# Optimization experiments

Hardware: AMD Instinct MI355X
Metric: run time of the kernel (lower is better)

Reference implementation:

```python
import jax, jax.numpy as jnp
import numpy as np

N_NODES = 50000
N_EDGES = 800000
NFEAT, NHID, IN_HEAD, NCLASS, OUT_HEAD = 256, 16, 8, 47, 1
NEG_SLOPE = 0.2


def setup_inputs() -> dict:
    key = jax.random.key(0)
    ks = jax.random.split(key, 10)
    x = jax.random.normal(ks[0], (N_NODES, NFEAT), dtype=jnp.float32)
    edge_index = jax.random.randint(ks[1], (2, N_EDGES), 0, N_NODES, dtype=jnp.int64)
    W1 = jax.random.normal(ks[2], (NFEAT, IN_HEAD * NHID), dtype=jnp.float32) * 0.06
    a1_src = jax.random.normal(ks[3], (IN_HEAD, NHID), dtype=jnp.float32) * 0.25
    a1_dst = jax.random.normal(ks[4], (IN_HEAD, NHID), dtype=jnp.float32) * 0.25
    b1 = jax.random.normal(ks[5], (IN_HEAD * NHID,), dtype=jnp.float32) * 0.02
    W2 = jax.random.normal(ks[6], (IN_HEAD * NHID, NCLASS), dtype=jnp.float32) * 0.09
    a2_src = jax.random.normal(ks[7], (OUT_HEAD, NCLASS), dtype=jnp.float32) * 0.15
    a2_dst = jax.random.normal(ks[8], (OUT_HEAD, NCLASS), dtype=jnp.float32) * 0.15
    b2 = jax.random.normal(ks[9], (NCLASS,), dtype=jnp.float32) * 0.02
    return {"x": x, "edge_index": edge_index, "W1": W1, "a1_src": a1_src,
            "a1_dst": a1_dst, "b1": b1, "W2": W2, "a2_src": a2_src,
            "a2_dst": a2_dst, "b2": b2}


def _gat_layer(x, W, a_src, a_dst, b, src, dst, n_nodes, concat):
    # x: [N, F_in]; W: [F_in, H*C]; a_*: [H, C]
    H, C = a_src.shape
    h = (x @ W).reshape(n_nodes, H, C)                        # [N, H, C]
    # per-node partial attention logits, then gather per edge
    s_src = jnp.einsum('nhc,hc->nh', h, a_src)                # [N, H]
    s_dst = jnp.einsum('nhc,hc->nh', h, a_dst)                # [N, H]
    e = jax.nn.leaky_relu(s_src[src] + s_dst[dst], NEG_SLOPE) # [E, H]
    # segment softmax over destination node
    m = jax.ops.segment_max(e, dst, num_segments=n_nodes)     # [N, H]
    ex = jnp.exp(e - m[dst])
    denom = jax.ops.segment_sum(ex, dst, num_segments=n_nodes)
    alpha = ex / (denom[dst] + 1e-16)                         # [E, H]
    # weighted message aggregation (scatter-add)
    msg = alpha[:, :, None] * h[src]                          # [E, H, C]
    out = jax.ops.segment_sum(msg, dst, num_segments=n_nodes) # [N, H, C]
    out = out.reshape(n_nodes, H * C) if concat else out.mean(axis=1)
    return out + b


def reference(x, edge_index, W1, a1_src, a1_dst, b1, W2, a2_src, a2_dst, b2):
    n = x.shape[0]
    # PyG GATConv default: add self-loops
    loops = jnp.arange(n, dtype=edge_index.dtype)
    src = jnp.concatenate([edge_index[0], loops])
    dst = jnp.concatenate([edge_index[1], loops])
    # eval mode: dropout is identity
    h = _gat_layer(x, W1, a1_src, a1_dst, b1, src, dst, n, concat=True)
    h = jax.nn.elu(h)
    out = _gat_layer(h, W2, a2_src, a2_dst, b2, src, dst, n, concat=False)
    return jax.nn.log_softmax(out, axis=1)
```

## Files before the change

### kernel.cpp

```cpp
#include <hip/hip_runtime.h>
#include <hip/hip_fp16.h>

#define N_NODES 50000
#define N_EDGES 800000
#define E2 (N_EDGES + N_NODES)

#define BSHIFT 6
#define BMASK 63
#define NBUCK 782
#define EPB 2048
#define NBLKC 416

typedef _Float16 h8v __attribute__((ext_vector_type(8)));
typedef float f4v __attribute__((ext_vector_type(4)));


__global__ __launch_bounds__(256) void k_hist(const int* __restrict__ ei,
        int* __restrict__ gh, const float* __restrict__ W1, _Float16* __restrict__ W1T,
        int* __restrict__ flag) {
    if (blockIdx.x == NBLKC) {
        if (threadIdx.x == 0) *flag = 0;
        for (int i = threadIdx.x; i < 128 * 256; i += 256) {
            int c = i >> 8, k = i & 255;
            W1T[i] = (_Float16)W1[k * 128 + c];
        }
        return;
    }
    __shared__ int h[NBUCK];
    int tid = threadIdx.x;
    for (int b = tid; b < NBUCK; b += 256) h[b] = 0;
    __syncthreads();
    int base = blockIdx.x * EPB;
    for (int i = tid; i < EPB; i += 256) {
        int e = base + i;
        if (e < E2) {
            int dst = (e < N_EDGES) ? ei[N_EDGES + e] : (e - N_EDGES);
            atomicAdd(&h[dst >> BSHIFT], 1);
        }
    }
    __syncthreads();
    for (int b = tid; b < NBUCK; b += 256) gh[blockIdx.x * NBUCK + b] = h[b];
}

__global__ __launch_bounds__(256) void k_colscan(int* __restrict__ gh,
        int* __restrict__ tot, int* __restrict__ boff, int* __restrict__ flag,
        const float* __restrict__ W2, float* __restrict__ W2p) {
    __shared__ int s_last;
    __shared__ int ws2[4];
    int wave = threadIdx.x >> 6, lane = threadIdx.x & 63;
    int b = blockIdx.x * 4 + wave;
    if (b < NBUCK) {
        int carry = 0;
        for (int c = 0; c < NBLKC; c += 64) {
            int k = c + lane;
            int v = (k < NBLKC) ? gh[k * NBUCK + b] : 0;
            int x = v;
            #pragma unroll
            for (int o = 1; o < 64; o <<= 1) { int y = __shfl_up(x, o); if (lane >= o) x += y; }
            if (k < NBLKC) gh[k * NBUCK + b] = carry + x - v;
            carry += __shfl(x, 63);
        }
        if (lane == 0) tot[b] = carry;
    }
    __syncthreads();
    if (threadIdx.x == 0) {
        __threadfence();
        int prev = atomicAdd(flag, 1);
        s_last = (prev == (int)gridDim.x - 1) ? 1 : 0;
    }
    __syncthreads();
    if (!s_last) return;
    __threadfence();
    int t = threadIdx.x;
    for (int i = t; i < 128 * 48; i += 256) {
        int k = i / 48, c = i - k * 48;
        W2p[i] = (c < 47) ? W2[k * 47 + c] : 0.f;
    }
    int v4[4]; int s = 0;
    #pragma unroll
    for (int j = 0; j < 4; ++j) {
        int b2 = t * 4 + j;
        v4[j] = (b2 < NBUCK) ? tot[b2] : 0;
        s += v4[j];
    }
    int x = s;
    #pragma unroll
    for (int o = 1; o < 64; o <<= 1) { int y = __shfl_up(x, o); if (lane >= o) x += y; }
    if (lane == 63) ws2[wave] = x;
    __syncthreads();
    int add = 0;
    for (int j = 0; j < wave; ++j) add += ws2[j];
    int run = add + x - s;
    #pragma unroll
    for (int j = 0; j < 4; ++j) {
        int b2 = t * 4 + j;
        if (b2 < NBUCK) boff[b2] = run;
        run += v4[j];
    }
    if (t == 255) boff[NBUCK] = run;
}

__global__ __launch_bounds__(256) void k_place(const int* __restrict__ ei,
        const int* __restrict__ gh, const int* __restrict__ boff,
        unsigned int* __restrict__ brec) {
    __shared__ int sbase[NBUCK];
    __shared__ int cnt[NBUCK];
    int tid = threadIdx.x;
    for (int b = tid; b < NBUCK; b += 256) {
        sbase[b] = boff[b] + gh[blockIdx.x * NBUCK + b];
        cnt[b] = 0;
    }
    __syncthreads();
    int base = blockIdx.x * EPB;
    for (int i = tid; i < EPB; i += 256) {
        int e = base + i;
        if (e < E2) {
            int src, dst;
            if (e < N_EDGES) { src = ei[e]; dst = ei[N_EDGES + e]; }
            else             { src = dst = e - N_EDGES; }
            int b = dst >> BSHIFT;
            int r = atomicAdd(&cnt[b], 1);
            brec[sbase[b] + r] = ((unsigned int)(dst & BMASK) << 16) | (unsigned int)src;
        }
    }
}

__global__ __launch_bounds__(256) void k_finalize(const unsigned int* __restrict__ brec,
        const int* __restrict__ boff, unsigned short* __restrict__ csr_src,
        int* __restrict__ offs) {
    int B = blockIdx.x;
    int tid = threadIdx.x;
    int base = boff[B];
    int total = boff[B + 1] - base;
    __shared__ int hist[64], cur[64];
    __shared__ unsigned short stage[2048];
    if (tid < 64) hist[tid] = 0;
    __syncthreads();
    const unsigned int* bp = brec + base;
    for (int i = tid; i < total; i += 256) atomicAdd(&hist[bp[i] >> 16], 1);
    __syncthreads();
    if (tid < 64) {
        int v = hist[tid];
        int x = v;
        #pragma unroll
        for (int o = 1; o < 64; o <<= 1) { int y = __shfl_up(x, o); if (tid >= o) x += y; }
        int excl = x - v;
        cur[tid] = excl;
        int n = B * 64 + tid;
        if (n < N_NODES) offs[n] = base + excl;
    }
    if (B == NBUCK - 1 && tid == 0) offs[N_NODES] = boff[NBUCK];
    __syncthreads();
    if (total <= 2048) {
        for (int i = tid; i < total; i += 256) {
            unsigned int r = bp[i];
            int p = atomicAdd(&cur[r >> 16], 1);
            stage[p] = (unsigned short)(r & 0xFFFFu);
        }
        __syncthreads();
        for (int i = tid; i < total; i += 256) csr_src[base + i] = stage[i];
    } else {
        for (int i = tid; i < total; i += 256) {
            unsigned int r = bp[i];
            int p = atomicAdd(&cur[r >> 16], 1);
            csr_src[base + p] = (unsigned short)(r & 0xFFFFu);
        }
    }
}


__global__ __launch_bounds__(128) void k_gemm1(const float* __restrict__ x,
        const _Float16* __restrict__ W1T, _Float16* __restrict__ h1h) {
    int lane = threadIdx.x & 63;
    int wv = threadIdx.x >> 6;
    int rowbase = blockIdx.x * 64 + wv * 32;
    int r0 = lane & 15;
    int kg = lane >> 4;
    f4v acc[2][8];
    #pragma unroll
    for (int i = 0; i < 2; ++i)
        #pragma unroll
        for (int j = 0; j < 8; ++j) acc[i][j] = (f4v)0.f;

    #pragma unroll 1
    for (int kt = 0; kt < 256; kt += 32) {
        h8v a[2];
        #pragma unroll
        for (int rf = 0; rf < 2; ++rf) {
            int row = rowbase + rf * 16 + r0;
            if (row >= N_NODES) row = N_NODES - 1;
            const float* ap = x + (size_t)row * 256 + kt + kg * 8;
            float4 lo = *(const float4*)ap;
            float4 hi = *(const float4*)(ap + 4);
            h8v t;
            t[0] = (_Float16)lo.x; t[1] = (_Float16)lo.y;
            t[2] = (_Float16)lo.z; t[3] = (_Float16)lo.w;
            t[4] = (_Float16)hi.x; t[5] = (_Float16)hi.y;
            t[6] = (_Float16)hi.z; t[7] = (_Float16)hi.w;
            a[rf] = t;
        }
        #pragma unroll
        for (int cf = 0; cf < 8; ++cf) {
            h8v b = *(const h8v*)(W1T + (size_t)(cf * 16 + r0) * 256 + kt + kg * 8);
            acc[0][cf] = __builtin_amdgcn_mfma_f32_16x16x32_f16(a[0], b, acc[0][cf], 0, 0, 0);
            acc[1][cf] = __builtin_amdgcn_mfma_f32_16x16x32_f16(a[1], b, acc[1][cf], 0, 0, 0);
        }
    }
    #pragma unroll
    for (int rf = 0; rf < 2; ++rf) {
        #pragma unroll
        for (int r = 0; r < 4; ++r) {
            int row = rowbase + rf * 16 + kg * 4 + r;
            if (row < N_NODES) {
                _Float16* orow = h1h + (size_t)row * 128 + r0;
                #pragma unroll
                for (int cf = 0; cf < 8; ++cf)
                    orow[cf * 16] = (_Float16)acc[rf][cf][r];
            }
        }
    }
}


__global__ void k_logits1(const __half* __restrict__ h1h,
                          const float* __restrict__ a1s, const float* __restrict__ a1d,
                          float* __restrict__ s1s, float* __restrict__ s1d) {
    int idx = blockIdx.x * blockDim.x + threadIdx.x;
    if (idx >= N_NODES * 8) return;
    int n = idx >> 3, h = idx & 7;
    const __half2* hp2 = (const __half2*)(h1h + (size_t)n * 128 + h * 16);
    float ss = 0.f, sd = 0.f;
    #pragma unroll
    for (int c2 = 0; c2 < 8; ++c2) {
        float2 v = __half22float2(hp2[c2]);
        ss += v.x * a1s[h * 16 + 2 * c2] + v.y * a1s[h * 16 + 2 * c2 + 1];
        sd += v.x * a1d[h * 16 + 2 * c2] + v.y * a1d[h * 16 + 2 * c2 + 1];
    }
    s1s[idx] = ss;
    s1d[idx] = sd;
}


__global__ __launch_bounds__(256) void k_agg1(const __half* __restrict__ h1h,
        const float* __restrict__ s1s, const float* __restrict__ s1d,
        const int* __restrict__ offs, const unsigned short* __restrict__ csr_src,
        const float* __restrict__ b1, __half* __restrict__ h2o) {
    int wave = threadIdx.x >> 6;
    int lane = threadIdx.x & 63;
    int n = blockIdx.x * 4 + wave;
    int beg = offs[n];
    int deg = offs[n + 1] - beg;

    int h = lane & 7;
    int slot = lane >> 3;
    int grp = lane >> 4;
    int cidx = lane & 15;
    int hc = cidx >> 1;
    float sdh = s1d[n * 8 + h];

    float dsum = 0.f;
    float acc[8] = {0.f, 0.f, 0.f, 0.f, 0.f, 0.f, 0.f, 0.f};
    for (int chunk = 0; chunk < deg; chunk += 16) {
        int i0 = chunk + slot;
        int i1 = chunk + 8 + slot;
        int e0 = csr_src[beg + ((i0 < deg) ? i0 : (deg - 1))];
        int e1 = csr_src[beg + ((i1 < deg) ? i1 : (deg - 1))];
        float a0 = 0.f, a1 = 0.f;
        if (i0 < deg) {
            float e = s1s[e0 * 8 + h] + sdh;
            e = (e > 0.f) ? e : 0.2f * e;
            a0 = __expf(e);
            dsum += a0;
        }
        if (i1 < deg) {
            float e = s1s[e1 * 8 + h] + sdh;
            e = (e > 0.f) ? e : 0.2f * e;
            a1 = __expf(e);
            dsum += a1;
        }
        int   s0 = __shfl(e0, grp * 8);       float w0 = __shfl(a0, grp * 8 + hc);
        int   s1 = __shfl(e0, (4 + grp) * 8); float w1 = __shfl(a0, (4 + grp) * 8 + hc);
        int   s2 = __shfl(e1, grp * 8);       float w2 = __shfl(a1, grp * 8 + hc);
        int   s3 = __shfl(e1, (4 + grp) * 8); float w3 = __shfl(a1, (4 + grp) * 8 + hc);
        h8v v0 = *(const h8v*)(h1h + (size_t)s0 * 128 + cidx * 8);
        h8v v1 = *(const h8v*)(h1h + (size_t)s1 * 128 + cidx * 8);
        h8v v2 = *(const h8v*)(h1h + (size_t)s2 * 128 + cidx * 8);
        h8v v3 = *(const h8v*)(h1h + (size_t)s3 * 128 + cidx * 8);
        #pragma unroll
        for (int j = 0; j < 8; ++j) acc[j] += w0 * (float)v0[j];
        #pragma unroll
        for (int j = 0; j < 8; ++j) acc[j] += w1 * (float)v1[j];
        #pragma unroll
        for (int j = 0; j < 8; ++j) acc[j] += w2 * (float)v2[j];
        #pragma unroll
        for (int j = 0; j < 8; ++j) acc[j] += w3 * (float)v3[j];
    }
    dsum += __shfl_xor(dsum, 8);
    dsum += __shfl_xor(dsum, 16);
    dsum += __shfl_xor(dsum, 32);
    float rd = 1.f / __shfl(dsum, hc);
    #pragma unroll
    for (int j = 0; j < 8; ++j) {
        acc[j] += __shfl_xor(acc[j], 16);
        acc[j] += __shfl_xor(acc[j], 32);
    }
    int c0 = cidx * 8 + grp * 2;
    float va = acc[grp * 2] * rd + b1[c0];
    va = (va > 0.f) ? va : (__expf(va) - 1.f);
    float vb = acc[grp * 2 + 1] * rd + b1[c0 + 1];
    vb = (vb > 0.f) ? vb : (__expf(vb) - 1.f);
    *(__half2*)(h2o + (size_t)n * 128 + c0) = __floats2half2_rn(va, vb);
}


__global__ __launch_bounds__(256) void k_gemm2(const __half* __restrict__ h2,
        const float* __restrict__ W2p,
        const float* __restrict__ a2s, const float* __restrict__ a2d,
        __half* __restrict__ g2h, float* __restrict__ s2s, float* __restrict__ s2d) {
    int n = blockIdx.x * 256 + threadIdx.x;
    bool valid = (n < N_NODES);
    int nn = valid ? n : (N_NODES - 1);
    const __half2* hrow = (const __half2*)(h2 + (size_t)nn * 128);
    float4 acc[12];
    #pragma unroll
    for (int j = 0; j < 12; ++j) acc[j] = make_float4(0.f, 0.f, 0.f, 0.f);
    #pragma unroll 1
    for (int k = 0; k < 128; k += 4) {
        float2 h01 = __half22float2(hrow[k / 2]);
        float2 h23 = __half22float2(hrow[k / 2 + 1]);
        float hk[4] = {h01.x, h01.y, h23.x, h23.y};
        #pragma unroll
        for (int kk = 0; kk < 4; ++kk) {
            const float* wrow = W2p + (size_t)(k + kk) * 48;
            #pragma unroll
            for (int j = 0; j < 12; ++j) {
                float4 wv = *(const float4*)(wrow + j * 4);
                acc[j].x += hk[kk] * wv.x;
                acc[j].y += hk[kk] * wv.y;
                acc[j].z += hk[kk] * wv.z;
                acc[j].w += hk[kk] * wv.w;
            }
        }
    }
    float vs = 0.f, vd = 0.f;
    #pragma unroll
    for (int j = 0; j < 12; ++j) {
        int c = j * 4;
        vs += acc[j].x * a2s[c + 0]; vd += acc[j].x * a2d[c + 0];
        vs += acc[j].y * a2s[c + 1]; vd += acc[j].y * a2d[c + 1];
        vs += acc[j].z * a2s[c + 2]; vd += acc[j].z * a2d[c + 2];
        if (j < 11) { vs += acc[j].w * a2s[c + 3]; vd += acc[j].w * a2d[c + 3]; }
    }
    if (valid) {
        __half2* orow = (__half2*)(g2h + (size_t)n * 48);
        #pragma unroll
        for (int j = 0; j < 12; ++j) {
            orow[j * 2 + 0] = __floats2half2_rn(acc[j].x, acc[j].y);
            orow[j * 2 + 1] = __floats2half2_rn(acc[j].z, acc[j].w);
        }
        s2s[n] = vs;
        s2d[n] = vd;
    }
}


__global__ __launch_bounds__(256) void k_agg2(const __half* __restrict__ g2h,
        const float* __restrict__ s2s, const float* __restrict__ s2d,
        const int* __restrict__ offs, const unsigned short* __restrict__ csr_src,
        const float* __restrict__ b2, float* __restrict__ outp) {
    int wave = threadIdx.x >> 6, lane = threadIdx.x & 63;
    int n = blockIdx.x * 4 + wave;
    int beg = offs[n];
    int deg = offs[n + 1] - beg;
    float sdn = s2d[n];
    int c = (lane < 47) ? lane : 47;

    float dsum = 0.f;
    float acc = 0.f;
    for (int chunk = 0; chunk < deg; chunk += 64) {
        int i = chunk + lane;
        int esrc = csr_src[beg + ((i < deg) ? i : (deg - 1))];
        float aN = 0.f;
        if (i < deg) {
            float e = s2s[esrc] + sdn;
            e = (e > 0.f) ? e : 0.2f * e;
            aN = __expf(e);
            dsum += aN;
        }
        int lim = deg - chunk; if (lim > 64) lim = 64;
        for (int g = 0; g < lim; g += 8) {
            int   srcs[8];
            float as[8];
            #pragma unroll
            for (int s = 0; s < 8; ++s) {
                srcs[s] = __shfl(esrc, g + s);
                as[s]   = __shfl(aN, g + s);
            }
            __half v[8];
            #pragma unroll
            for (int s = 0; s < 8; ++s) v[s] = g2h[(size_t)srcs[s] * 48 + c];
            #pragma unroll
            for (int s = 0; s < 8; ++s) acc += as[s] * __half2float(v[s]);
        }
    }
    #pragma unroll
    for (int o = 32; o; o >>= 1) dsum += __shfl_xor(dsum, o);
    acc *= 1.f / dsum;

    float l = (lane < 47) ? acc + b2[lane] : -1e30f;
    float rm = l;
    #pragma unroll
    for (int o = 32; o; o >>= 1) rm = fmaxf(rm, __shfl_xor(rm, o));
    float p = (lane < 47) ? __expf(l - rm) : 0.f;
    float ps = p;
    #pragma unroll
    for (int o = 32; o; o >>= 1) ps += __shfl_xor(ps, o);
    float lse = rm + __logf(ps);
    if (lane < 47) outp[(size_t)n * 47 + lane] = l - lse;
}


extern "C" void kernel_launch(void* const* d_in, const int* in_sizes, int n_in,
                              void* d_out, int out_size, void* d_ws, size_t ws_size,
                              hipStream_t stream) {
    const float* x   = (const float*)d_in[0];
    const int*   ei  = (const int*)d_in[1];
    const float* W1  = (const float*)d_in[2];
    const float* a1s = (const float*)d_in[3];
    const float* a1d = (const float*)d_in[4];
    const float* b1  = (const float*)d_in[5];
    const float* W2  = (const float*)d_in[6];
    const float* a2s = (const float*)d_in[7];
    const float* a2d = (const float*)d_in[8];
    const float* b2  = (const float*)d_in[9];
    float* outp = (float*)d_out;

    char* ws = (char*)d_ws;
    size_t off = 0;
    auto alloc = [&](size_t bytes) -> void* {
        void* p = ws + off;
        off += (bytes + 255) & ~(size_t)255;
        return p;
    };
    int* gh      = (int*)alloc((size_t)NBLKC * NBUCK * 4);
    int* tot     = (int*)alloc((size_t)NBUCK * 4);
    int* boff    = (int*)alloc((size_t)(NBUCK + 1) * 4);
    int* flag    = (int*)alloc(256);
    unsigned int* brec = (unsigned int*)alloc((size_t)E2 * 4);
    unsigned short* csr_src = (unsigned short*)alloc((size_t)E2 * 2);
    int* offs    = (int*)alloc((size_t)(N_NODES + 1) * 4);
    __half* h1h  = (__half*)alloc((size_t)N_NODES * 128 * 2);
    float* s1s   = (float*)alloc((size_t)N_NODES * 8 * 4);
    float* s1d   = (float*)alloc((size_t)N_NODES * 8 * 4);
    __half* h2h  = (__half*)alloc((size_t)N_NODES * 128 * 2);
    __half* g2h  = (__half*)alloc((size_t)N_NODES * 48 * 2);
    float* s2s   = (float*)alloc((size_t)N_NODES * 4);
    float* s2d   = (float*)alloc((size_t)N_NODES * 4);
    float* W2p   = (float*)alloc((size_t)128 * 48 * 4);
    _Float16* W1T = (_Float16*)alloc((size_t)128 * 256 * 2);

    (void)in_sizes; (void)n_in; (void)out_size; (void)ws_size;

    k_hist<<<NBLKC + 1, 256, 0, stream>>>(ei, gh, W1, W1T, flag);
    k_colscan<<<(NBUCK + 3) / 4, 256, 0, stream>>>(gh, tot, boff, flag, W2, W2p);
    k_place<<<NBLKC, 256, 0, stream>>>(ei, gh, boff, brec);
    k_finalize<<<NBUCK, 256, 0, stream>>>(brec, boff, csr_src, offs);

    k_gemm1<<<(N_NODES + 63) / 64, 128, 0, stream>>>(x, W1T, (_Float16*)h1h);
    k_logits1<<<(N_NODES * 8 + 255) / 256, 256, 0, stream>>>(h1h, a1s, a1d, s1s, s1d);
    k_agg1<<<N_NODES / 4, 256, 0, stream>>>(h1h, s1s, s1d, offs, csr_src, b1, h2h);

    k_gemm2<<<(N_NODES + 255) / 256, 256, 0, stream>>>(h2h, W2p, a2s, a2d, g2h, s2s, s2d);
    k_agg2<<<N_NODES / 4, 256, 0, stream>>>(g2h, s2s, s2d, offs, csr_src, b2, outp);
}
```

Before: 193.6 us.

## Co-schedule CSR build with GEMM1 and logits, halve histogram blocks, skip empty agg1 slots

Result: faster. 181.0 us (-6.5%).

```diff
diff --git a/kernel.cpp b/kernel.cpp
--- a/kernel.cpp
+++ b/kernel.cpp
@@ -8,18 +8,18 @@
 #define BSHIFT 6
 #define BMASK 63
 #define NBUCK 782
-#define EPB 2048
-#define NBLKC 416
+#define EPB 4096
+#define NBLKC 208
+#define CSBLK 196
+#define G1BLK 391
 
 typedef _Float16 h8v __attribute__((ext_vector_type(8)));
 typedef float f4v __attribute__((ext_vector_type(4)));
 
 
 __global__ __launch_bounds__(256) void k_hist(const int* __restrict__ ei,
-        int* __restrict__ gh, const float* __restrict__ W1, _Float16* __restrict__ W1T,
-        int* __restrict__ flag) {
+        int* __restrict__ gh, const float* __restrict__ W1, _Float16* __restrict__ W1T) {
     if (blockIdx.x == NBLKC) {
-        if (threadIdx.x == 0) *flag = 0;
         for (int i = threadIdx.x; i < 128 * 256; i += 256) {
             int c = i >> 8, k = i & 255;
             W1T[i] = (_Float16)W1[k * 128 + c];
@@ -42,138 +42,30 @@
     for (int b = tid; b < NBUCK; b += 256) gh[blockIdx.x * NBUCK + b] = h[b];
 }
 
-__global__ __launch_bounds__(256) void k_colscan(int* __restrict__ gh,
-        int* __restrict__ tot, int* __restrict__ boff, int* __restrict__ flag,
-        const float* __restrict__ W2, float* __restrict__ W2p) {
-    __shared__ int s_last;
-    __shared__ int ws2[4];
-    int wave = threadIdx.x >> 6, lane = threadIdx.x & 63;
-    int b = blockIdx.x * 4 + wave;
-    if (b < NBUCK) {
+__global__ __launch_bounds__(256) void k_csg(int* __restrict__ gh,
+        int* __restrict__ tot, const float* __restrict__ x,
+        const _Float16* __restrict__ W1T, _Float16* __restrict__ h1h) {
+    if (blockIdx.x < CSBLK) {
+        int wave = threadIdx.x >> 6, lane = threadIdx.x & 63;
+        int b = blockIdx.x * 4 + wave;
+        if (b >= NBUCK) return;
         int carry = 0;
         for (int c = 0; c < NBLKC; c += 64) {
             int k = c + lane;
             int v = (k < NBLKC) ? gh[k * NBUCK + b] : 0;
-            int x = v;
-            #pragma unroll
-            for (int o = 1; o < 64; o <<= 1) { int y = __shfl_up(x, o); if (lane >= o) x += y; }
-            if (k < NBLKC) gh[k * NBUCK + b] = carry + x - v;
-            carry += __shfl(x, 63);
+            int xv = v;
+            #pragma unroll
+            for (int o = 1; o < 64; o <<= 1) { int y = __shfl_up(xv, o); if (lane >= o) xv += y; }
+            if (k < NBLKC) gh[k * NBUCK + b] = carry + xv - v;
+            carry += __shfl(xv, 63);
         }
         if (lane == 0) tot[b] = carry;
-    }
-    __syncthreads();
-    if (threadIdx.x == 0) {
-        __threadfence();
-        int prev = atomicAdd(flag, 1);
-        s_last = (prev == (int)gridDim.x - 1) ? 1 : 0;
-    }
-    __syncthreads();
-    if (!s_last) return;
-    __threadfence();
-    int t = threadIdx.x;
-    for (int i = t; i < 128 * 48; i += 256) {
-        int k = i / 48, c = i - k * 48;
-        W2p[i] = (c < 47) ? W2[k * 47 + c] : 0.f;
-    }
-    int v4[4]; int s = 0;
-    #pragma unroll
-    for (int j = 0; j < 4; ++j) {
-        int b2 = t * 4 + j;
-        v4[j] = (b2 < NBUCK) ? tot[b2] : 0;
-        s += v4[j];
-    }
-    int x = s;
-    #pragma unroll
-    for (int o = 1; o < 64; o <<= 1) { int y = __shfl_up(x, o); if (lane >= o) x += y; }
-    if (lane == 63) ws2[wave] = x;
-    __syncthreads();
-    int add = 0;
-    for (int j = 0; j < wave; ++j) add += ws2[j];
-    int run = add + x - s;
-    #pragma unroll
-    for (int j = 0; j < 4; ++j) {
-        int b2 = t * 4 + j;
-        if (b2 < NBUCK) boff[b2] = run;
-        run += v4[j];
-    }
-    if (t == 255) boff[NBUCK] = run;
-}
-
-__global__ __launch_bounds__(256) void k_place(const int* __restrict__ ei,
-        const int* __restrict__ gh, const int* __restrict__ boff,
-        unsigned int* __restrict__ brec) {
-    __shared__ int sbase[NBUCK];
-    __shared__ int cnt[NBUCK];
-    int tid = threadIdx.x;
-    for (int b = tid; b < NBUCK; b += 256) {
-        sbase[b] = boff[b] + gh[blockIdx.x * NBUCK + b];
-        cnt[b] = 0;
-    }
-    __syncthreads();
-    int base = blockIdx.x * EPB;
-    for (int i = tid; i < EPB; i += 256) {
-        int e = base + i;
-        if (e < E2) {
-            int src, dst;
-            if (e < N_EDGES) { src = ei[e]; dst = ei[N_EDGES + e]; }
-            else             { src = dst = e - N_EDGES; }
-            int b = dst >> BSHIFT;
-            int r = atomicAdd(&cnt[b], 1);
-            brec[sbase[b] + r] = ((unsigned int)(dst & BMASK) << 16) | (unsigned int)src;
-        }
-    }
-}
-
-__global__ __launch_bounds__(256) void k_finalize(const unsigned int* __restrict__ brec,
-        const int* __restrict__ boff, unsigned short* __restrict__ csr_src,
-        int* __restrict__ offs) {
-    int B = blockIdx.x;
-    int tid = threadIdx.x;
-    int base = boff[B];
-    int total = boff[B + 1] - base;
-    __shared__ int hist[64], cur[64];
-    __shared__ unsigned short stage[2048];
-    if (tid < 64) hist[tid] = 0;
-    __syncthreads();
-    const unsigned int* bp = brec + base;
-    for (int i = tid; i < total; i += 256) atomicAdd(&hist[bp[i] >> 16], 1);
-    __syncthreads();
-    if (tid < 64) {
-        int v = hist[tid];
-        int x = v;
-        #pragma unroll
-        for (int o = 1; o < 64; o <<= 1) { int y = __shfl_up(x, o); if (tid >= o) x += y; }
-        int excl = x - v;
-        cur[tid] = excl;
-        int n = B * 64 + tid;
-        if (n < N_NODES) offs[n] = base + excl;
-    }
-    if (B == NBUCK - 1 && tid == 0) offs[N_NODES] = boff[NBUCK];
-    __syncthreads();
-    if (total <= 2048) {
-        for (int i = tid; i < total; i += 256) {
-            unsigned int r = bp[i];
-            int p = atomicAdd(&cur[r >> 16], 1);
-            stage[p] = (unsigned short)(r & 0xFFFFu);
-        }
-        __syncthreads();
-        for (int i = tid; i < total; i += 256) csr_src[base + i] = stage[i];
-    } else {
-        for (int i = tid; i < total; i += 256) {
-            unsigned int r = bp[i];
-            int p = atomicAdd(&cur[r >> 16], 1);
-            csr_src[base + p] = (unsigned short)(r & 0xFFFFu);
-        }
-    }
-}
-
-
-__global__ __launch_bounds__(128) void k_gemm1(const float* __restrict__ x,
-        const _Float16* __restrict__ W1T, _Float16* __restrict__ h1h) {
+        return;
+    }
+    int gblk = blockIdx.x - CSBLK;
     int lane = threadIdx.x & 63;
     int wv = threadIdx.x >> 6;
-    int rowbase = blockIdx.x * 64 + wv * 32;
+    int rowbase = gblk * 128 + wv * 32;
     int r0 = lane & 15;
     int kg = lane >> 4;
     f4v acc[2][8];
@@ -221,11 +113,44 @@
     }
 }
 
-
-__global__ void k_logits1(const __half* __restrict__ h1h,
-                          const float* __restrict__ a1s, const float* __restrict__ a1d,
-                          float* __restrict__ s1s, float* __restrict__ s1d) {
-    int idx = blockIdx.x * blockDim.x + threadIdx.x;
+__global__ __launch_bounds__(256) void k_mid(const int* __restrict__ tot,
+        int* __restrict__ boff, const float* __restrict__ W2, float* __restrict__ W2p,
+        const __half* __restrict__ h1h,
+        const float* __restrict__ a1s, const float* __restrict__ a1d,
+        float* __restrict__ s1s, float* __restrict__ s1d) {
+    if (blockIdx.x == 0) {
+        int t = threadIdx.x;
+        for (int i = t; i < 128 * 48; i += 256) {
+            int k = i / 48, c = i - k * 48;
+            W2p[i] = (c < 47) ? W2[k * 47 + c] : 0.f;
+        }
+        int v4[4]; int s = 0;
+        #pragma unroll
+        for (int j = 0; j < 4; ++j) {
+            int b2 = t * 4 + j;
+            v4[j] = (b2 < NBUCK) ? tot[b2] : 0;
+            s += v4[j];
+        }
+        int lane = t & 63, w = t >> 6;
+        __shared__ int ws[4];
+        int xv = s;
+        #pragma unroll
+        for (int o = 1; o < 64; o <<= 1) { int y = __shfl_up(xv, o); if (lane >= o) xv += y; }
+        if (lane == 63) ws[w] = xv;
+        __syncthreads();
+        int add = 0;
+        for (int j = 0; j < w; ++j) add += ws[j];
+        int run = add + xv - s;
+        #pragma unroll
+        for (int j = 0; j < 4; ++j) {
+            int b2 = t * 4 + j;
+            if (b2 < NBUCK) boff[b2] = run;
+            run += v4[j];
+        }
+        if (t == 255) boff[NBUCK] = run;
+        return;
+    }
+    int idx = (blockIdx.x - 1) * 256 + threadIdx.x;
     if (idx >= N_NODES * 8) return;
     int n = idx >> 3, h = idx & 7;
     const __half2* hp2 = (const __half2*)(h1h + (size_t)n * 128 + h * 16);
@@ -238,6 +163,74 @@
     }
     s1s[idx] = ss;
     s1d[idx] = sd;
+}
+
+__global__ __launch_bounds__(256) void k_place(const int* __restrict__ ei,
+        const int* __restrict__ gh, const int* __restrict__ boff,
+        unsigned int* __restrict__ brec) {
+    __shared__ int sbase[NBUCK];
+    __shared__ int cnt[NBUCK];
+    int tid = threadIdx.x;
+    for (int b = tid; b < NBUCK; b += 256) {
+        sbase[b] = boff[b] + gh[blockIdx.x * NBUCK + b];
+        cnt[b] = 0;
+    }
+    __syncthreads();
+    int base = blockIdx.x * EPB;
+    for (int i = tid; i < EPB; i += 256) {
+        int e = base + i;
+        if (e < E2) {
+            int src, dst;
+            if (e < N_EDGES) { src = ei[e]; dst = ei[N_EDGES + e]; }
+            else             { src = dst = e - N_EDGES; }
+            int b = dst >> BSHIFT;
+            int r = atomicAdd(&cnt[b], 1);
+            brec[sbase[b] + r] = ((unsigned int)(dst & BMASK) << 16) | (unsigned int)src;
+        }
+    }
+}
+
+__global__ __launch_bounds__(256) void k_finalize(const unsigned int* __restrict__ brec,
+        const int* __restrict__ boff, unsigned short* __restrict__ csr_src,
+        int* __restrict__ offs) {
+    int B = blockIdx.x;
+    int tid = threadIdx.x;
+    int base = boff[B];
+    int total = boff[B + 1] - base;
+    __shared__ int hist[64], cur[64];
+    __shared__ unsigned short stage[2048];
+    if (tid < 64) hist[tid] = 0;
+    __syncthreads();
+    const unsigned int* bp = brec + base;
+    for (int i = tid; i < total; i += 256) atomicAdd(&hist[bp[i] >> 16], 1);
+    __syncthreads();
+    if (tid < 64) {
+        int v = hist[tid];
+        int x = v;
+        #pragma unroll
+        for (int o = 1; o < 64; o <<= 1) { int y = __shfl_up(x, o); if (tid >= o) x += y; }
+        int excl = x - v;
+        cur[tid] = excl;
+        int n = B * 64 + tid;
+        if (n < N_NODES) offs[n] = base + excl;
+    }
+    if (B == NBUCK - 1 && tid == 0) offs[N_NODES] = boff[NBUCK];
+    __syncthreads();
+    if (total <= 2048) {
+        for (int i = tid; i < total; i += 256) {
+            unsigned int r = bp[i];
+            int p = atomicAdd(&cur[r >> 16], 1);
+            stage[p] = (unsigned short)(r & 0xFFFFu);
+        }
+        __syncthreads();
+        for (int i = tid; i < total; i += 256) csr_src[base + i] = stage[i];
+    } else {
+        for (int i = tid; i < total; i += 256) {
+            unsigned int r = bp[i];
+            int p = atomicAdd(&cur[r >> 16], 1);
+            csr_src[base + p] = (unsigned short)(r & 0xFFFFu);
+        }
+    }
 }
 
 
@@ -261,39 +254,55 @@
     float dsum = 0.f;
     float acc[8] = {0.f, 0.f, 0.f, 0.f, 0.f, 0.f, 0.f, 0.f};
     for (int chunk = 0; chunk < deg; chunk += 16) {
+        int rem = deg - chunk; if (rem > 16) rem = 16;
         int i0 = chunk + slot;
-        int i1 = chunk + 8 + slot;
         int e0 = csr_src[beg + ((i0 < deg) ? i0 : (deg - 1))];
-        int e1 = csr_src[beg + ((i1 < deg) ? i1 : (deg - 1))];
-        float a0 = 0.f, a1 = 0.f;
+        float a0 = 0.f;
         if (i0 < deg) {
             float e = s1s[e0 * 8 + h] + sdh;
             e = (e > 0.f) ? e : 0.2f * e;
             a0 = __expf(e);
             dsum += a0;
         }
-        if (i1 < deg) {
-            float e = s1s[e1 * 8 + h] + sdh;
-            e = (e > 0.f) ? e : 0.2f * e;
-            a1 = __expf(e);
-            dsum += a1;
-        }
-        int   s0 = __shfl(e0, grp * 8);       float w0 = __shfl(a0, grp * 8 + hc);
-        int   s1 = __shfl(e0, (4 + grp) * 8); float w1 = __shfl(a0, (4 + grp) * 8 + hc);
-        int   s2 = __shfl(e1, grp * 8);       float w2 = __shfl(a1, grp * 8 + hc);
-        int   s3 = __shfl(e1, (4 + grp) * 8); float w3 = __shfl(a1, (4 + grp) * 8 + hc);
-        h8v v0 = *(const h8v*)(h1h + (size_t)s0 * 128 + cidx * 8);
-        h8v v1 = *(const h8v*)(h1h + (size_t)s1 * 128 + cidx * 8);
-        h8v v2 = *(const h8v*)(h1h + (size_t)s2 * 128 + cidx * 8);
-        h8v v3 = *(const h8v*)(h1h + (size_t)s3 * 128 + cidx * 8);
-        #pragma unroll
-        for (int j = 0; j < 8; ++j) acc[j] += w0 * (float)v0[j];
-        #pragma unroll
-        for (int j = 0; j < 8; ++j) acc[j] += w1 * (float)v1[j];
-        #pragma unroll
-        for (int j = 0; j < 8; ++j) acc[j] += w2 * (float)v2[j];
-        #pragma unroll
-        for (int j = 0; j < 8; ++j) acc[j] += w3 * (float)v3[j];
+        {
+            int   s0 = __shfl(e0, grp * 8);
+            float w0 = __shfl(a0, grp * 8 + hc);
+            h8v v0 = *(const h8v*)(h1h + (size_t)s0 * 128 + cidx * 8);
+            #pragma unroll
+            for (int j = 0; j < 8; ++j) acc[j] += w0 * (float)v0[j];
+        }
+        if (rem > 4) {
+            int   s1 = __shfl(e0, (4 + grp) * 8);
+            float w1 = __shfl(a0, (4 + grp) * 8 + hc);
+            h8v v1 = *(const h8v*)(h1h + (size_t)s1 * 128 + cidx * 8);
+            #pragma unroll
+            for (int j = 0; j < 8; ++j) acc[j] += w1 * (float)v1[j];
+        }
+        if (rem > 8) {
+            int i1 = chunk + 8 + slot;
+            int e1 = csr_src[beg + ((i1 < deg) ? i1 : (deg - 1))];
+            float a1 = 0.f;
+            if (i1 < deg) {
+                float e = s1s[e1 * 8 + h] + sdh;
+                e = (e > 0.f) ? e : 0.2f * e;
+                a1 = __expf(e);
+                dsum += a1;
+            }
+            {
+                int   s2 = __shfl(e1, grp * 8);
+                float w2 = __shfl(a1, grp * 8 + hc);
+                h8v v2 = *(const h8v*)(h1h + (size_t)s2 * 128 + cidx * 8);
+                #pragma unroll
+                for (int j = 0; j < 8; ++j) acc[j] += w2 * (float)v2[j];
+            }
+            if (rem > 12) {
+                int   s3 = __shfl(e1, (4 + grp) * 8);
+                float w3 = __shfl(a1, (4 + grp) * 8 + hc);
+                h8v v3 = *(const h8v*)(h1h + (size_t)s3 * 128 + cidx * 8);
+                #pragma unroll
+                for (int j = 0; j < 8; ++j) acc[j] += w3 * (float)v3[j];
+            }
+        }
     }
     dsum += __shfl_xor(dsum, 8);
     dsum += __shfl_xor(dsum, 16);
@@ -445,7 +454,6 @@
     int* gh      = (int*)alloc((size_t)NBLKC * NBUCK * 4);
     int* tot     = (int*)alloc((size_t)NBUCK * 4);
     int* boff    = (int*)alloc((size_t)(NBUCK + 1) * 4);
-    int* flag    = (int*)alloc(256);
     unsigned int* brec = (unsigned int*)alloc((size_t)E2 * 4);
     unsigned short* csr_src = (unsigned short*)alloc((size_t)E2 * 2);
     int* offs    = (int*)alloc((size_t)(N_NODES + 1) * 4);
@@ -461,15 +469,14 @@
 
     (void)in_sizes; (void)n_in; (void)out_size; (void)ws_size;
 
-    k_hist<<<NBLKC + 1, 256, 0, stream>>>(ei, gh, W1, W1T, flag);
-    k_colscan<<<(NBUCK + 3) / 4, 256, 0, stream>>>(gh, tot, boff, flag, W2, W2p);
+    k_hist<<<NBLKC + 1, 256, 0, stream>>>(ei, gh, W1, W1T);
+    k_csg<<<CSBLK + G1BLK, 256, 0, stream>>>(gh, tot, x, W1T, (_Float16*)h1h);
+    k_mid<<<1 + (N_NODES * 8 + 255) / 256, 256, 0, stream>>>(tot, boff, W2, W2p,
+                                                             h1h, a1s, a1d, s1s, s1d);
     k_place<<<NBLKC, 256, 0, stream>>>(ei, gh, boff, brec);
     k_finalize<<<NBUCK, 256, 0, stream>>>(brec, boff, csr_src, offs);
 
-    k_gemm1<<<(N_NODES + 63) / 64, 128, 0, stream>>>(x, W1T, (_Float16*)h1h);
-    k_logits1<<<(N_NODES * 8 + 255) / 256, 256, 0, stream>>>(h1h, a1s, a1d, s1s, s1d);
     k_agg1<<<N_NODES / 4, 256, 0, stream>>>(h1h, s1s, s1d, offs, csr_src, b1, h2h);
-
     k_gemm2<<<(N_NODES + 255) / 256, 256, 0, stream>>>(h2h, W2p, a2s, a2d, g2h, s2s, s2d);
     k_agg2<<<N_NODES / 4, 256, 0, stream>>>(g2h, s2s, s2d, offs, csr_src, b2, outp);
 }
```
